# Kernel optimization log

Measured on AMD Instinct MI355X. Metric: run time of the kernel, lower is better.

## Reference

```python
import jax, jax.numpy as jnp
import numpy as np

E = 500_000
NODE_DIM = 128
EDGE_DIM = 128
GLOB_DIM = 64
NUM_GRAPHS = 64
HIDDEN = 4 * EDGE_DIM  # 512
IN_DIM = 2 * NODE_DIM + EDGE_DIM + GLOB_DIM  # 448
EPS = 1e-5


def setup_inputs() -> dict:
    key = jax.random.key(0)
    ks = jax.random.split(key, 12)
    src = jax.random.normal(ks[0], (E, NODE_DIM), dtype=jnp.float32)
    dest = jax.random.normal(ks[1], (E, NODE_DIM), dtype=jnp.float32)
    edge_attr = jax.random.normal(ks[2], (E, EDGE_DIM), dtype=jnp.float32)
    u = jax.random.normal(ks[3], (NUM_GRAPHS, GLOB_DIM), dtype=jnp.float32)
    batch = jnp.sort(jax.random.randint(ks[4], (E,), 0, NUM_GRAPHS, dtype=jnp.int32))
    # MLP params (kaiming-ish scale)
    W1 = jax.random.normal(ks[5], (IN_DIM, HIDDEN), dtype=jnp.float32) / np.sqrt(IN_DIM)
    b1 = jnp.zeros((HIDDEN,), dtype=jnp.float32)
    W2 = jax.random.normal(ks[6], (HIDDEN, EDGE_DIM), dtype=jnp.float32) / np.sqrt(HIDDEN)
    b2 = jnp.zeros((EDGE_DIM,), dtype=jnp.float32)
    # GraphNorm params
    gn_weight = jnp.ones((EDGE_DIM,), dtype=jnp.float32)
    gn_bias = jnp.zeros((EDGE_DIM,), dtype=jnp.float32)
    mean_scale = jnp.ones((EDGE_DIM,), dtype=jnp.float32)
    return {"src": src, "dest": dest, "edge_attr": edge_attr, "u": u, "batch": batch,
            "W1": W1, "b1": b1, "W2": W2, "b2": b2,
            "gn_weight": gn_weight, "gn_bias": gn_bias, "mean_scale": mean_scale}


def _graph_norm(x, batch, weight, bias, mean_scale):
    # per-graph mean
    cnt = jax.ops.segment_sum(jnp.ones((x.shape[0],), x.dtype), batch, num_segments=NUM_GRAPHS)
    cnt = jnp.maximum(cnt, 1.0)[:, None]  # [G,1]
    mean = jax.ops.segment_sum(x, batch, num_segments=NUM_GRAPHS) / cnt  # [G,D]
    out = x - mean[batch] * mean_scale
    var = jax.ops.segment_sum(out * out, batch, num_segments=NUM_GRAPHS) / cnt  # [G,D]
    std = jnp.sqrt(var + EPS)
    return out / std[batch] * weight + bias


def reference(src, dest, edge_attr, u, batch, W1, b1, W2, b2, gn_weight, gn_bias, mean_scale):
    # gather per-graph globals + concat: [E, 2*node+edge+glob]
    h = jnp.concatenate([src, dest, edge_attr, u[batch]], axis=1)
    h = jax.nn.relu(h @ W1 + b1) @ W2 + b2  # [E, edge_dim]
    out = _graph_norm(h + edge_attr, batch, gn_weight, gn_bias, mean_scale)
    return out  # dropout is identity in eval / p=0.0
```

## Files before the change

kernel.cpp:

```cpp
#include <hip/hip_runtime.h>
#include <stdint.h>

#define E_EDGES   500000
#define MBLK      32
#define NBLK      15625
#define EPSV      1e-5f

typedef unsigned short u16;
typedef __attribute__((ext_vector_type(8))) short short8;
typedef __attribute__((ext_vector_type(4))) float f32x4;

__device__ __forceinline__ u16 f2bf(float f) {
  uint32_t u = __float_as_uint(f);
  u += 0x7fffu + ((u >> 16) & 1u);
  return (u16)(u >> 16);
}

__global__ void prep_weights(const float* __restrict__ W1, const float* __restrict__ W2,
                             u16* __restrict__ w1f, u16* __restrict__ w2f) {
  int idx = blockIdx.x * blockDim.x + threadIdx.x;
  if (idx < 32*14*64) {
    int lane = idx & 63; int t = idx >> 6; int k32 = t % 14; int n16 = t / 14;
    int n = n16*16 + (lane & 15); int k0 = k32*32 + (lane >> 4)*8;
    short8 pk;
#pragma unroll
    for (int j = 0; j < 8; ++j) pk[j] = (short)f2bf(W1[(size_t)(k0 + j)*512 + n]);
    *(short8*)&w1f[(size_t)idx * 8] = pk;
  } else if (idx < 32*14*64 + 8*16*64) {
    int i2 = idx - 32*14*64;
    int lane = i2 & 63; int t = i2 >> 6; int k32 = t % 16; int n16 = t / 16;
    int n = n16*16 + (lane & 15); int k0 = k32*32 + (lane >> 4)*8;
    short8 pk;
#pragma unroll
    for (int j = 0; j < 8; ++j) pk[j] = (short)f2bf(W2[(size_t)(k0 + j)*128 + n]);
    *(short8*)&w2f[(size_t)i2 * 8] = pk;
  }
}

#define SWZ16(row, byte) ((byte) ^ (((row) & 7) << 4))

__global__ __launch_bounds__(256, 4)
void fused_kernel(const float* __restrict__ srcp, const float* __restrict__ destp,
                  const float* __restrict__ edgep, const float* __restrict__ up,
                  const int* __restrict__ batch, const float* __restrict__ b1,
                  const float* __restrict__ b2,
                  const u16* __restrict__ w1f, const u16* __restrict__ w2f,
                  float* __restrict__ outp,
                  float* __restrict__ sums0, float* __restrict__ sums2,
                  float* __restrict__ cntsh, int nshard) {
  const int tid  = threadIdx.x;
  const int lane = tid & 63;
  const int w    = tid >> 6;
  const int l15  = lane & 15, l4 = lane >> 4;

  __shared__ __align__(16) u16 lds[32*512];
  char* ldsb = (char*)lds;

  const long grow0 = (long)blockIdx.x * MBLK;

  {
    const int srow = tid >> 3;
    const int c8   = (tid & 7) * 8;
    const long sgrow = grow0 + srow;
    const int  bat = batch[sgrow];
#pragma unroll
    for (int j = 0; j < 7; ++j) {
      const float* sp;
      if (j == 0)      sp = srcp  + sgrow*128 + c8;
      else if (j == 1) sp = srcp  + sgrow*128 + 64 + c8;
      else if (j == 2) sp = destp + sgrow*128 + c8;
      else if (j == 3) sp = destp + sgrow*128 + 64 + c8;
      else if (j == 4) sp = edgep + sgrow*128 + c8;
      else if (j == 5) sp = edgep + sgrow*128 + 64 + c8;
      else             sp = up + (size_t)bat*64 + c8;
      f32x4 t0 = *(const f32x4*)(sp);
      f32x4 t1 = *(const f32x4*)(sp + 4);
      short8 pk;
      pk[0]=(short)f2bf(t0[0]); pk[1]=(short)f2bf(t0[1]);
      pk[2]=(short)f2bf(t0[2]); pk[3]=(short)f2bf(t0[3]);
      pk[4]=(short)f2bf(t1[0]); pk[5]=(short)f2bf(t1[1]);
      pk[6]=(short)f2bf(t1[2]); pk[7]=(short)f2bf(t1[3]);
      *(short8*)(ldsb + srow*896 + SWZ16(srow, (j*64 + c8)*2)) = pk;
    }
  }
  __syncthreads();

  f32x4 acc1[2][8];
#pragma unroll
  for (int mi = 0; mi < 2; ++mi)
#pragma unroll
    for (int nj = 0; nj < 8; ++nj) {
      float bv = b1[w*128 + nj*16 + l15];
      acc1[mi][nj] = (f32x4){bv, bv, bv, bv};
    }

#pragma unroll 2
  for (int k32 = 0; k32 < 14; ++k32) {
    short8 a[2], b[8];
#pragma unroll
    for (int mi = 0; mi < 2; ++mi) {
      int row = mi*16 + l15;
      a[mi] = *(const short8*)(ldsb + row*896 + SWZ16(row, k32*64 + l4*16));
    }
#pragma unroll
    for (int nj = 0; nj < 8; ++nj) {
      int n16 = w*8 + nj;
      b[nj] = *(const short8*)&w1f[((size_t)(n16*14 + k32)*64 + lane)*8];
    }
#pragma unroll
    for (int mi = 0; mi < 2; ++mi)
#pragma unroll
      for (int nj = 0; nj < 8; ++nj)
        acc1[mi][nj] = __builtin_amdgcn_mfma_f32_16x16x32_bf16(a[mi], b[nj], acc1[mi][nj], 0, 0, 0);
  }
  __syncthreads();

#pragma unroll
  for (int nj = 0; nj < 8; ++nj) {
    int n = w*128 + nj*16 + l15;
#pragma unroll
    for (int mi = 0; mi < 2; ++mi)
#pragma unroll
      for (int rr = 0; rr < 4; ++rr) {
        int row = mi*16 + l4*4 + rr;
        *(u16*)(ldsb + row*1024 + SWZ16(row, n*2)) = f2bf(fmaxf(acc1[mi][nj][rr], 0.f));
      }
  }
  __syncthreads();

  const int c4    = tid & 31;
  const int rbase = tid >> 5;
  f32x4 ebuf[4];
#pragma unroll
  for (int p = 0; p < 4; ++p)
    ebuf[p] = *(const f32x4*)(edgep + (grow0 + rbase + p*8)*128 + c4*4);

  f32x4 acc2[2][2];
#pragma unroll
  for (int nj = 0; nj < 2; ++nj) {
    float bv = b2[w*32 + nj*16 + l15];
    acc2[0][nj] = (f32x4){bv, bv, bv, bv};
    acc2[1][nj] = (f32x4){bv, bv, bv, bv};
  }

#pragma unroll 4
  for (int kb = 0; kb < 16; ++kb) {
    short8 a2[2], bf[2];
#pragma unroll
    for (int mi = 0; mi < 2; ++mi) {
      int row = mi*16 + l15;
      a2[mi] = *(const short8*)(ldsb + row*1024 + SWZ16(row, kb*64 + l4*16));
    }
#pragma unroll
    for (int nj = 0; nj < 2; ++nj) {
      int n16 = w*2 + nj;
      bf[nj] = *(const short8*)&w2f[(((size_t)(n16*16 + kb))*64 + lane)*8];
    }
#pragma unroll
    for (int mi = 0; mi < 2; ++mi)
#pragma unroll
      for (int nj = 0; nj < 2; ++nj)
        acc2[mi][nj] = __builtin_amdgcn_mfma_f32_16x16x32_bf16(a2[mi], bf[nj], acc2[mi][nj], 0, 0, 0);
  }
  __syncthreads();

#pragma unroll
  for (int mi = 0; mi < 2; ++mi)
#pragma unroll
    for (int nj = 0; nj < 2; ++nj) {
      int col = w*32 + nj*16 + l15;
#pragma unroll
      for (int rr = 0; rr < 4; ++rr) {
        int row = mi*16 + l4*4 + rr;
        *(float*)(ldsb + row*512 + SWZ16(row, col*4)) = acc2[mi][nj][rr];
      }
    }
  __syncthreads();

  const int g0 = batch[grow0];
  const int g1 = batch[grow0 + MBLK - 1];
  const int sh = blockIdx.x & (nshard - 1);

  if (g0 == g1) {
    f32x4 s = (f32x4){0,0,0,0}, s2 = (f32x4){0,0,0,0};
#pragma unroll
    for (int p = 0; p < 4; ++p) {
      int row = rbase + p*8;
      f32x4 y = *(const f32x4*)(ldsb + row*512 + SWZ16(row, c4*16));
      y = y + ebuf[p];
      *(f32x4*)(outp + (grow0 + row)*128 + c4*4) = y;
      s = s + y; s2 = s2 + y*y;
    }
    int slot = 16384 + (rbase*32 + c4)*32;
    *(f32x4*)(ldsb + slot)      = s;
    *(f32x4*)(ldsb + slot + 16) = s2;
    __syncthreads();
    int c4r = tid >> 3, stat = (tid >> 2) & 1, cq = tid & 3;
    float v = 0.f;
#pragma unroll
    for (int r = 0; r < 8; ++r)
      v += *(const float*)(ldsb + 16384 + (r*32 + c4r)*32 + stat*16 + cq*4);
    float* dst = stat ? sums2 : sums0;
    atomicAdd(&dst[(size_t)sh*8192 + g0*128 + c4r*4 + cq], v);
    if (tid == 0) atomicAdd(&cntsh[sh*64 + g0], (float)MBLK);
  } else {
    f32x4 s = (f32x4){0,0,0,0}, s2 = (f32x4){0,0,0,0};
    float rc = 0.f; int gcur = -1;
#pragma unroll
    for (int p = 0; p < 4; ++p) {
      int row = rbase + p*8;
      int g = batch[grow0 + row];
      if (g != gcur) {
        if (gcur >= 0) {
#pragma unroll
          for (int c = 0; c < 4; ++c) {
            atomicAdd(&sums0[(size_t)sh*8192 + gcur*128 + c4*4 + c], s[c]);
            atomicAdd(&sums2[(size_t)sh*8192 + gcur*128 + c4*4 + c], s2[c]);
          }
          if (c4 == 0) atomicAdd(&cntsh[sh*64 + gcur], rc);
        }
        gcur = g; s = (f32x4){0,0,0,0}; s2 = (f32x4){0,0,0,0}; rc = 0.f;
      }
      f32x4 y = *(const f32x4*)(ldsb + row*512 + SWZ16(row, c4*16));
      y = y + ebuf[p];
      *(f32x4*)(outp + (grow0 + row)*128 + c4*4) = y;
      s = s + y; s2 = s2 + y*y; rc += 1.f;
    }
#pragma unroll
    for (int c = 0; c < 4; ++c) {
      atomicAdd(&sums0[(size_t)sh*8192 + gcur*128 + c4*4 + c], s[c]);
      atomicAdd(&sums2[(size_t)sh*8192 + gcur*128 + c4*4 + c], s2[c]);
    }
    if (c4 == 0) atomicAdd(&cntsh[sh*64 + gcur], rc);
  }
}

__global__ void finalize_kernel(const float* __restrict__ sums0, const float* __restrict__ sums2,
                                const float* __restrict__ cntsh, int nshard,
                                const float* __restrict__ gnw, const float* __restrict__ gnb,
                                const float* __restrict__ ms,
                                float* __restrict__ scale, float* __restrict__ shift) {
  int idx = blockIdx.x*blockDim.x + threadIdx.x;
  if (idx >= 64*128) return;
  int g = idx >> 7, d = idx & 127;
  float s = 0.f, s2 = 0.f, c = 0.f;
  for (int sh = 0; sh < nshard; ++sh) {
    s  += sums0[(size_t)sh*8192 + idx];
    s2 += sums2[(size_t)sh*8192 + idx];
    c  += cntsh[sh*64 + g];
  }
  c = fmaxf(c, 1.0f);
  float mean = s / c;
  float mm = mean * ms[d];
  float var = fmaxf(s2 / c - 2.f*mm*mean + mm*mm, 0.f);
  float sc = gnw[d] / sqrtf(var + EPSV);
  scale[idx] = sc;
  shift[idx] = gnb[d] - mm*sc;
}

__global__ void norm_kernel(float* __restrict__ y, const int* __restrict__ batch,
                            const float* __restrict__ scale, const float* __restrict__ shift) {
  long i = (long)blockIdx.x*blockDim.x + threadIdx.x;
  const long n4 = (long)E_EDGES * 32;
  long stride = (long)gridDim.x*blockDim.x;
  for (; i < n4; i += stride) {
    long row = i >> 5;
    int dq = (int)(i & 31) << 2;
    int g = batch[row];
    f32x4 v = *(f32x4*)(y + i*4);
    f32x4 sc = *(const f32x4*)(scale + g*128 + dq);
    f32x4 sh = *(const f32x4*)(shift + g*128 + dq);
    v = v*sc + sh;
    *(f32x4*)(y + i*4) = v;
  }
}

extern "C" void kernel_launch(void* const* d_in, const int* in_sizes, int n_in,
                              void* d_out, int out_size, void* d_ws, size_t ws_size,
                              hipStream_t stream) {
  const float* srcp  = (const float*)d_in[0];
  const float* destp = (const float*)d_in[1];
  const float* edgep = (const float*)d_in[2];
  const float* up    = (const float*)d_in[3];
  const int*   batch = (const int*)d_in[4];
  const float* W1    = (const float*)d_in[5];
  const float* b1    = (const float*)d_in[6];
  const float* W2    = (const float*)d_in[7];
  const float* b2    = (const float*)d_in[8];
  const float* gnw   = (const float*)d_in[9];
  const float* gnb   = (const float*)d_in[10];
  const float* ms    = (const float*)d_in[11];
  float* outp = (float*)d_out;

  char* ws = (char*)d_ws;
  u16*   w1f   = (u16*)(ws + 0);
  u16*   w2f   = (u16*)(ws + 458752);
  float* scale = (float*)(ws + 589824);
  float* shift = (float*)(ws + 622592);
  float* cntsh = (float*)(ws + 655360);
  int nshard = 32;
  while (nshard > 1 && 663552 + (size_t)nshard*65536 > ws_size) nshard >>= 1;
  float* sums0 = (float*)(ws + 663552);
  float* sums2 = (float*)(ws + 663552 + (size_t)nshard*32768);

  hipMemsetAsync(ws + 655360, 0, 8192 + (size_t)nshard*65536, stream);
  prep_weights<<<dim3(144), dim3(256), 0, stream>>>(W1, W2, w1f, w2f);

  fused_kernel<<<dim3(NBLK), dim3(256), 0, stream>>>(srcp, destp, edgep, up, batch,
                                                     b1, b2, w1f, w2f, outp,
                                                     sums0, sums2, cntsh, nshard);

  finalize_kernel<<<dim3(32), dim3(256), 0, stream>>>(sums0, sums2, cntsh, nshard,
                                                      gnw, gnb, ms, scale, shift);
  norm_kernel<<<dim3(2048), dim3(256), 0, stream>>>(outp, batch, scale, shift);
}
```

Before: 577.4 us.

## Make fused MLP kernel persistent with software-prefetched next-tile inputs

Turns the fused edge-MLP kernel into a persistent kernel with a fixed grid of 768 blocks, each looping over 32-row tiles. The next tile's input rows are loaded into registers during the current tile's epilogue and written to LDS after the second GEMM, so global load latency overlaps with MFMA work. LDS is split into separate regions for the output and stats staging to allow this. Occupancy hint drops from 4 to 3 blocks per CU to make room for the extra prefetch registers. The bf16 conversion also switches to the library intrinsic with packed 32-bit LDS stores.

```diff
diff --git a/kernel.cpp b/kernel.cpp
--- a/kernel.cpp
+++ b/kernel.cpp
@@ -1,19 +1,26 @@
 #include <hip/hip_runtime.h>
+#include <hip/hip_bf16.h>
 #include <stdint.h>
 
 #define E_EDGES   500000
 #define MBLK      32
-#define NBLK      15625
+#define NT        15625
+#define GRIDP     768
 #define EPSV      1e-5f
+#define YOFF      28672
+#define STOFF     45056
 
 typedef unsigned short u16;
 typedef __attribute__((ext_vector_type(8))) short short8;
 typedef __attribute__((ext_vector_type(4))) float f32x4;
+typedef __attribute__((ext_vector_type(2))) uint32_t u32x2;
 
 __device__ __forceinline__ u16 f2bf(float f) {
-  uint32_t u = __float_as_uint(f);
-  u += 0x7fffu + ((u >> 16) & 1u);
-  return (u16)(u >> 16);
+  __hip_bfloat16 h = __float2bfloat16(f);
+  return *(u16*)&h;
+}
+__device__ __forceinline__ uint32_t pk2bf(float lo, float hi) {
+  return (uint32_t)f2bf(lo) | ((uint32_t)f2bf(hi) << 16);
 }
 
 __global__ void prep_weights(const float* __restrict__ W1, const float* __restrict__ W2,
@@ -39,7 +46,7 @@
 
 #define SWZ16(row, byte) ((byte) ^ (((row) & 7) << 4))
 
-__global__ __launch_bounds__(256, 4)
+__global__ __launch_bounds__(256, 3)
 void fused_kernel(const float* __restrict__ srcp, const float* __restrict__ destp,
                   const float* __restrict__ edgep, const float* __restrict__ up,
                   const int* __restrict__ batch, const float* __restrict__ b1,
@@ -53,15 +60,17 @@
   const int w    = tid >> 6;
   const int l15  = lane & 15, l4 = lane >> 4;
 
-  __shared__ __align__(16) u16 lds[32*512];
-  char* ldsb = (char*)lds;
-
-  const long grow0 = (long)blockIdx.x * MBLK;
+  __shared__ __align__(16) char ldsb[53248];
+
+  const int srow = tid >> 3;
+  const int c8   = (tid & 7) * 8;
+  const int c4    = tid & 31;
+  const int rbase = tid >> 5;
+
+  int t = blockIdx.x;
 
   {
-    const int srow = tid >> 3;
-    const int c8   = (tid & 7) * 8;
-    const long sgrow = grow0 + srow;
+    const long sgrow = (long)t*MBLK + srow;
     const int  bat = batch[sgrow];
 #pragma unroll
     for (int j = 0; j < 7; ++j) {
@@ -75,163 +84,192 @@
       else             sp = up + (size_t)bat*64 + c8;
       f32x4 t0 = *(const f32x4*)(sp);
       f32x4 t1 = *(const f32x4*)(sp + 4);
-      short8 pk;
-      pk[0]=(short)f2bf(t0[0]); pk[1]=(short)f2bf(t0[1]);
-      pk[2]=(short)f2bf(t0[2]); pk[3]=(short)f2bf(t0[3]);
-      pk[4]=(short)f2bf(t1[0]); pk[5]=(short)f2bf(t1[1]);
-      pk[6]=(short)f2bf(t1[2]); pk[7]=(short)f2bf(t1[3]);
-      *(short8*)(ldsb + srow*896 + SWZ16(srow, (j*64 + c8)*2)) = pk;
+      u32x2 lohi0 = (u32x2){pk2bf(t0[0], t0[1]), pk2bf(t0[2], t0[3])};
+      u32x2 lohi1 = (u32x2){pk2bf(t1[0], t1[1]), pk2bf(t1[2], t1[3])};
+      char* dst = ldsb + srow*896 + SWZ16(srow, (j*64 + c8)*2);
+      *(u32x2*)(dst)     = lohi0;
+      *(u32x2*)(dst + 8) = lohi1;
     }
   }
   __syncthreads();
 
-  f32x4 acc1[2][8];
-#pragma unroll
-  for (int mi = 0; mi < 2; ++mi)
+  for (;;) {
+    const long grow0 = (long)t * MBLK;
+    const int  nt = t + GRIDP;
+    const bool hasnext = nt < NT;
+
+    f32x4 acc1[2][8];
 #pragma unroll
     for (int nj = 0; nj < 8; ++nj) {
-      float bv = b1[w*128 + nj*16 + l15];
-      acc1[mi][nj] = (f32x4){bv, bv, bv, bv};
+      float bv = b1[(w*8 + nj)*16 + l15];
+      acc1[0][nj] = (f32x4){bv, bv, bv, bv};
+      acc1[1][nj] = (f32x4){bv, bv, bv, bv};
     }
 
 #pragma unroll 2
-  for (int k32 = 0; k32 < 14; ++k32) {
-    short8 a[2], b[8];
-#pragma unroll
-    for (int mi = 0; mi < 2; ++mi) {
-      int row = mi*16 + l15;
-      a[mi] = *(const short8*)(ldsb + row*896 + SWZ16(row, k32*64 + l4*16));
-    }
+    for (int k32 = 0; k32 < 14; ++k32) {
+      short8 a[2], b[8];
+#pragma unroll
+      for (int mi = 0; mi < 2; ++mi) {
+        int row = mi*16 + l15;
+        a[mi] = *(const short8*)(ldsb + row*896 + SWZ16(row, k32*64 + l4*16));
+      }
+#pragma unroll
+      for (int nj = 0; nj < 8; ++nj)
+        b[nj] = *(const short8*)&w1f[((size_t)((w*8 + nj)*14 + k32)*64 + lane)*8];
+#pragma unroll
+      for (int mi = 0; mi < 2; ++mi)
+#pragma unroll
+        for (int nj = 0; nj < 8; ++nj)
+          acc1[mi][nj] = __builtin_amdgcn_mfma_f32_16x16x32_bf16(a[mi], b[nj], acc1[mi][nj], 0, 0, 0);
+    }
+    __syncthreads();
+
+    f32x4 xn[14];
+    if (hasnext) {
+      const long nrow = (long)nt*MBLK + srow;
+      const int  nbat = batch[nrow];
+#pragma unroll
+      for (int j = 0; j < 7; ++j) {
+        const float* sp;
+        if (j == 0)      sp = srcp  + nrow*128 + c8;
+        else if (j == 1) sp = srcp  + nrow*128 + 64 + c8;
+        else if (j == 2) sp = destp + nrow*128 + c8;
+        else if (j == 3) sp = destp + nrow*128 + 64 + c8;
+        else if (j == 4) sp = edgep + nrow*128 + c8;
+        else if (j == 5) sp = edgep + nrow*128 + 64 + c8;
+        else             sp = up + (size_t)nbat*64 + c8;
+        xn[j*2]   = *(const f32x4*)(sp);
+        xn[j*2+1] = *(const f32x4*)(sp + 4);
+      }
+    }
+    f32x4 ebuf[4];
+#pragma unroll
+    for (int p = 0; p < 4; ++p)
+      ebuf[p] = *(const f32x4*)(edgep + (grow0 + rbase + p*8)*128 + c4*4);
+
 #pragma unroll
     for (int nj = 0; nj < 8; ++nj) {
-      int n16 = w*8 + nj;
-      b[nj] = *(const short8*)&w1f[((size_t)(n16*14 + k32)*64 + lane)*8];
-    }
+      int n = (w*8 + nj)*16 + l15;
+#pragma unroll
+      for (int mi = 0; mi < 2; ++mi)
+#pragma unroll
+        for (int rr = 0; rr < 4; ++rr) {
+          int row = mi*16 + l4*4 + rr;
+          *(u16*)(ldsb + row*1024 + SWZ16(row, n*2)) = f2bf(fmaxf(acc1[mi][nj][rr], 0.f));
+        }
+    }
+    __syncthreads();
+
+    f32x4 acc2[2][2];
+#pragma unroll
+    for (int nj = 0; nj < 2; ++nj) {
+      float bv = b2[(w*2 + nj)*16 + l15];
+      acc2[0][nj] = (f32x4){bv, bv, bv, bv};
+      acc2[1][nj] = (f32x4){bv, bv, bv, bv};
+    }
+
+#pragma unroll 4
+    for (int kb = 0; kb < 16; ++kb) {
+      short8 hb[2], wfr[2];
+#pragma unroll
+      for (int mi = 0; mi < 2; ++mi) {
+        int row = mi*16 + l15;
+        hb[mi] = *(const short8*)(ldsb + row*1024 + SWZ16(row, kb*64 + l4*16));
+      }
+#pragma unroll
+      for (int nj = 0; nj < 2; ++nj)
+        wfr[nj] = *(const short8*)&w2f[(((size_t)((w*2 + nj)*16 + kb))*64 + lane)*8];
+#pragma unroll
+      for (int mi = 0; mi < 2; ++mi)
+#pragma unroll
+        for (int nj = 0; nj < 2; ++nj)
+          acc2[mi][nj] = __builtin_amdgcn_mfma_f32_16x16x32_bf16(hb[mi], wfr[nj], acc2[mi][nj], 0, 0, 0);
+    }
+    __syncthreads();
+
 #pragma unroll
     for (int mi = 0; mi < 2; ++mi)
 #pragma unroll
-      for (int nj = 0; nj < 8; ++nj)
-        acc1[mi][nj] = __builtin_amdgcn_mfma_f32_16x16x32_bf16(a[mi], b[nj], acc1[mi][nj], 0, 0, 0);
-  }
-  __syncthreads();
-
-#pragma unroll
-  for (int nj = 0; nj < 8; ++nj) {
-    int n = w*128 + nj*16 + l15;
-#pragma unroll
-    for (int mi = 0; mi < 2; ++mi)
-#pragma unroll
-      for (int rr = 0; rr < 4; ++rr) {
-        int row = mi*16 + l4*4 + rr;
-        *(u16*)(ldsb + row*1024 + SWZ16(row, n*2)) = f2bf(fmaxf(acc1[mi][nj][rr], 0.f));
-      }
-  }
-  __syncthreads();
-
-  const int c4    = tid & 31;
-  const int rbase = tid >> 5;
-  f32x4 ebuf[4];
-#pragma unroll
-  for (int p = 0; p < 4; ++p)
-    ebuf[p] = *(const f32x4*)(edgep + (grow0 + rbase + p*8)*128 + c4*4);
-
-  f32x4 acc2[2][2];
-#pragma unroll
-  for (int nj = 0; nj < 2; ++nj) {
-    float bv = b2[w*32 + nj*16 + l15];
-    acc2[0][nj] = (f32x4){bv, bv, bv, bv};
-    acc2[1][nj] = (f32x4){bv, bv, bv, bv};
-  }
-
-#pragma unroll 4
-  for (int kb = 0; kb < 16; ++kb) {
-    short8 a2[2], bf[2];
-#pragma unroll
-    for (int mi = 0; mi < 2; ++mi) {
-      int row = mi*16 + l15;
-      a2[mi] = *(const short8*)(ldsb + row*1024 + SWZ16(row, kb*64 + l4*16));
-    }
-#pragma unroll
-    for (int nj = 0; nj < 2; ++nj) {
-      int n16 = w*2 + nj;
-      bf[nj] = *(const short8*)&w2f[(((size_t)(n16*16 + kb))*64 + lane)*8];
-    }
-#pragma unroll
-    for (int mi = 0; mi < 2; ++mi)
-#pragma unroll
-      for (int nj = 0; nj < 2; ++nj)
-        acc2[mi][nj] = __builtin_amdgcn_mfma_f32_16x16x32_bf16(a2[mi], bf[nj], acc2[mi][nj], 0, 0, 0);
-  }
-  __syncthreads();
-
-#pragma unroll
-  for (int mi = 0; mi < 2; ++mi)
-#pragma unroll
-    for (int nj = 0; nj < 2; ++nj) {
-      int col = w*32 + nj*16 + l15;
-#pragma unroll
-      for (int rr = 0; rr < 4; ++rr) {
-        int row = mi*16 + l4*4 + rr;
-        *(float*)(ldsb + row*512 + SWZ16(row, col*4)) = acc2[mi][nj][rr];
-      }
-    }
-  __syncthreads();
-
-  const int g0 = batch[grow0];
-  const int g1 = batch[grow0 + MBLK - 1];
-  const int sh = blockIdx.x & (nshard - 1);
-
-  if (g0 == g1) {
-    f32x4 s = (f32x4){0,0,0,0}, s2 = (f32x4){0,0,0,0};
-#pragma unroll
-    for (int p = 0; p < 4; ++p) {
-      int row = rbase + p*8;
-      f32x4 y = *(const f32x4*)(ldsb + row*512 + SWZ16(row, c4*16));
-      y = y + ebuf[p];
-      *(f32x4*)(outp + (grow0 + row)*128 + c4*4) = y;
-      s = s + y; s2 = s2 + y*y;
-    }
-    int slot = 16384 + (rbase*32 + c4)*32;
-    *(f32x4*)(ldsb + slot)      = s;
-    *(f32x4*)(ldsb + slot + 16) = s2;
+      for (int nj = 0; nj < 2; ++nj) {
+        int col = (w*2 + nj)*16 + l15;
+#pragma unroll
+        for (int rr = 0; rr < 4; ++rr) {
+          int row = mi*16 + l4*4 + rr;
+          *(float*)(ldsb + YOFF + row*512 + SWZ16(row, col*4)) = acc2[mi][nj][rr];
+        }
+      }
+    if (hasnext) {
+#pragma unroll
+      for (int j = 0; j < 7; ++j) {
+        u32x2 lohi0 = (u32x2){pk2bf(xn[j*2][0],   xn[j*2][1]),   pk2bf(xn[j*2][2],   xn[j*2][3])};
+        u32x2 lohi1 = (u32x2){pk2bf(xn[j*2+1][0], xn[j*2+1][1]), pk2bf(xn[j*2+1][2], xn[j*2+1][3])};
+        char* dst = ldsb + srow*896 + SWZ16(srow, (j*64 + c8)*2);
+        *(u32x2*)(dst)     = lohi0;
+        *(u32x2*)(dst + 8) = lohi1;
+      }
+    }
     __syncthreads();
-    int c4r = tid >> 3, stat = (tid >> 2) & 1, cq = tid & 3;
-    float v = 0.f;
-#pragma unroll
-    for (int r = 0; r < 8; ++r)
-      v += *(const float*)(ldsb + 16384 + (r*32 + c4r)*32 + stat*16 + cq*4);
-    float* dst = stat ? sums2 : sums0;
-    atomicAdd(&dst[(size_t)sh*8192 + g0*128 + c4r*4 + cq], v);
-    if (tid == 0) atomicAdd(&cntsh[sh*64 + g0], (float)MBLK);
-  } else {
-    f32x4 s = (f32x4){0,0,0,0}, s2 = (f32x4){0,0,0,0};
-    float rc = 0.f; int gcur = -1;
-#pragma unroll
-    for (int p = 0; p < 4; ++p) {
-      int row = rbase + p*8;
-      int g = batch[grow0 + row];
-      if (g != gcur) {
-        if (gcur >= 0) {
-#pragma unroll
-          for (int c = 0; c < 4; ++c) {
-            atomicAdd(&sums0[(size_t)sh*8192 + gcur*128 + c4*4 + c], s[c]);
-            atomicAdd(&sums2[(size_t)sh*8192 + gcur*128 + c4*4 + c], s2[c]);
+
+    const int g0 = batch[grow0];
+    const int g1 = batch[grow0 + MBLK - 1];
+    const int sh = t & (nshard - 1);
+
+    if (g0 == g1) {
+      f32x4 s = (f32x4){0,0,0,0}, s2 = (f32x4){0,0,0,0};
+#pragma unroll
+      for (int p = 0; p < 4; ++p) {
+        int row = rbase + p*8;
+        f32x4 y = *(const f32x4*)(ldsb + YOFF + row*512 + SWZ16(row, c4*16));
+        y = y + ebuf[p];
+        *(f32x4*)(outp + (grow0 + row)*128 + c4*4) = y;
+        s = s + y; s2 = s2 + y*y;
+      }
+      int slot = STOFF + (rbase*32 + c4)*32;
+      *(f32x4*)(ldsb + slot)      = s;
+      *(f32x4*)(ldsb + slot + 16) = s2;
+      __syncthreads();
+      int c4r = tid >> 3, stat = (tid >> 2) & 1, cq = tid & 3;
+      float v = 0.f;
+#pragma unroll
+      for (int r = 0; r < 8; ++r)
+        v += *(const float*)(ldsb + STOFF + (r*32 + c4r)*32 + stat*16 + cq*4);
+      float* dst = stat ? sums2 : sums0;
+      atomicAdd(&dst[(size_t)sh*8192 + g0*128 + c4r*4 + cq], v);
+      if (tid == 0) atomicAdd(&cntsh[sh*64 + g0], (float)MBLK);
+    } else {
+      f32x4 s = (f32x4){0,0,0,0}, s2 = (f32x4){0,0,0,0};
+      float rc = 0.f; int gcur = -1;
+#pragma unroll
+      for (int p = 0; p < 4; ++p) {
+        int row = rbase + p*8;
+        int g = batch[grow0 + row];
+        if (g != gcur) {
+          if (gcur >= 0) {
+#pragma unroll
+            for (int c = 0; c < 4; ++c) {
+              atomicAdd(&sums0[(size_t)sh*8192 + gcur*128 + c4*4 + c], s[c]);
+              atomicAdd(&sums2[(size_t)sh*8192 + gcur*128 + c4*4 + c], s2[c]);
+            }
+            if (c4 == 0) atomicAdd(&cntsh[sh*64 + gcur], rc);
           }
-          if (c4 == 0) atomicAdd(&cntsh[sh*64 + gcur], rc);
+          gcur = g; s = (f32x4){0,0,0,0}; s2 = (f32x4){0,0,0,0}; rc = 0.f;
         }
-        gcur = g; s = (f32x4){0,0,0,0}; s2 = (f32x4){0,0,0,0}; rc = 0.f;
-      }
-      f32x4 y = *(const f32x4*)(ldsb + row*512 + SWZ16(row, c4*16));
-      y = y + ebuf[p];
-      *(f32x4*)(outp + (grow0 + row)*128 + c4*4) = y;
-      s = s + y; s2 = s2 + y*y; rc += 1.f;
-    }
-#pragma unroll
-    for (int c = 0; c < 4; ++c) {
-      atomicAdd(&sums0[(size_t)sh*8192 + gcur*128 + c4*4 + c], s[c]);
-      atomicAdd(&sums2[(size_t)sh*8192 + gcur*128 + c4*4 + c], s2[c]);
-    }
-    if (c4 == 0) atomicAdd(&cntsh[sh*64 + gcur], rc);
+        f32x4 y = *(const f32x4*)(ldsb + YOFF + row*512 + SWZ16(row, c4*16));
+        y = y + ebuf[p];
+        *(f32x4*)(outp + (grow0 + row)*128 + c4*4) = y;
+        s = s + y; s2 = s2 + y*y; rc += 1.f;
+      }
+#pragma unroll
+      for (int c = 0; c < 4; ++c) {
+        atomicAdd(&sums0[(size_t)sh*8192 + gcur*128 + c4*4 + c], s[c]);
+        atomicAdd(&sums2[(size_t)sh*8192 + gcur*128 + c4*4 + c], s2[c]);
+      }
+      if (c4 == 0) atomicAdd(&cntsh[sh*64 + gcur], rc);
+    }
+
+    if (!hasnext) break;
+    t = nt;
   }
 }
 
@@ -306,9 +344,9 @@
   hipMemsetAsync(ws + 655360, 0, 8192 + (size_t)nshard*65536, stream);
   prep_weights<<<dim3(144), dim3(256), 0, stream>>>(W1, W2, w1f, w2f);
 
-  fused_kernel<<<dim3(NBLK), dim3(256), 0, stream>>>(srcp, destp, edgep, up, batch,
-                                                     b1, b2, w1f, w2f, outp,
-                                                     sums0, sums2, cntsh, nshard);
+  fused_kernel<<<dim3(GRIDP), dim3(256), 0, stream>>>(srcp, destp, edgep, up, batch,
+                                                      b1, b2, w1f, w2f, outp,
+                                                      sums0, sums2, cntsh, nshard);
 
   finalize_kernel<<<dim3(32), dim3(256), 0, stream>>>(sums0, sums2, cntsh, nshard,
                                                       gnw, gnb, ms, scale, shift);
```

After: 1.272 ms. 2.2x slower.
